# Kernel optimization log

Hardware: AMD Instinct MI355X
Metric: run time of the kernel (lower is better)

Reference implementation:

```python
import jax, jax.numpy as jnp
import numpy as np

B, L, H, N, NB = 16, 4096, 256, 64, 4
EXPAND = 2


def setup_inputs() -> dict:
    key = jax.random.key(0)
    ks = jax.random.split(key, 12)
    def nrm(k, shape, scale):
        return jax.random.normal(k, shape, dtype=jnp.float32) * scale
    inp = {}
    inp["x"] = jax.random.normal(ks[0], (B, L, 1), dtype=jnp.float32)
    # conv stem: Conv1d(1 -> H, kernel 5, pad 2)
    inp["conv_w"] = nrm(ks[1], (H, 1, 5), 1.0 / np.sqrt(5.0))
    inp["conv_b"] = jnp.zeros((H,), jnp.float32)
    # per-block S4 (S4D diagonal kernel) params, stacked over NB blocks
    inp["s4_norm_w"] = jnp.ones((NB, H), jnp.float32)
    inp["s4_norm_b"] = jnp.zeros((NB, H), jnp.float32)
    inp["log_dt"] = (np.log(0.001) + jax.random.uniform(ks[2], (NB, H), dtype=jnp.float32) * (np.log(0.1) - np.log(0.001))).astype(jnp.float32)
    inp["log_A_real"] = jnp.full((NB, H, N), np.log(0.5), jnp.float32)
    inp["A_imag"] = jnp.tile(np.pi * jnp.arange(N, dtype=jnp.float32), (NB, H, 1))
    inp["C_re"] = nrm(ks[3], (NB, H, N), 0.5 ** 0.5)
    inp["C_im"] = nrm(ks[4], (NB, H, N), 0.5 ** 0.5)
    inp["D"] = nrm(ks[5], (NB, H), 1.0)
    # S4 output GLU linear: H -> 2H, then glu -> H
    inp["s4_out_w"] = nrm(ks[6], (NB, 2 * H, H), 1.0 / np.sqrt(H))
    inp["s4_out_b"] = jnp.zeros((NB, 2 * H), jnp.float32)
    # FF block (expand=2)
    inp["ff_norm_w"] = jnp.ones((NB, H), jnp.float32)
    inp["ff_norm_b"] = jnp.zeros((NB, H), jnp.float32)
    inp["ff_w1"] = nrm(ks[7], (NB, EXPAND * H, H), 1.0 / np.sqrt(H))
    inp["ff_b1"] = jnp.zeros((NB, EXPAND * H), jnp.float32)
    inp["ff_w2"] = nrm(ks[8], (NB, H, EXPAND * H), 1.0 / np.sqrt(EXPAND * H))
    inp["ff_b2"] = jnp.zeros((NB, H), jnp.float32)
    return inp


def _ln_ch(x, w, b):
    # LayerNorm over channel dim of x: [B, H, L] (prenorm on transposed layout)
    mu = jnp.mean(x, axis=1, keepdims=True)
    var = jnp.mean((x - mu) ** 2, axis=1, keepdims=True)
    return (x - mu) * jax.lax.rsqrt(var + 1e-5) * w[None, :, None] + b[None, :, None]


def _s4d_kernel(log_dt, log_A_real, A_imag, C_re, C_im, Lk):
    # Diagonal SSM (S4D) convolution kernel, returns [H, Lk]
    dt = jnp.exp(log_dt)                       # [H]
    A = -jnp.exp(log_A_real) + 1j * A_imag     # [H, N]
    dtA = A * dt[:, None]                      # [H, N]
    C = (C_re + 1j * C_im) * (jnp.exp(dtA) - 1.0) / A
    V = jnp.exp(dtA[:, :, None] * jnp.arange(Lk, dtype=jnp.float32))  # [H, N, Lk]
    return 2.0 * jnp.einsum('hn,hnl->hl', C, V).real


def reference(x, conv_w, conv_b, s4_norm_w, s4_norm_b, log_dt, log_A_real, A_imag,
              C_re, C_im, D, s4_out_w, s4_out_b, ff_norm_w, ff_norm_b,
              ff_w1, ff_b1, ff_w2, ff_b2):
    u = jnp.transpose(x, (0, 2, 1))  # [B, 1, L]
    h = jax.lax.conv_general_dilated(u, conv_w, (1,), [(2, 2)],
                                     dimension_numbers=('NCH', 'OIH', 'NCH'))
    h = h + conv_b[None, :, None]    # [B, H, L]
    Lx = h.shape[-1]
    for i in range(NB):
        # --- S4 residual block (prenorm, FFT long conv, D-skip, GELU, GLU out) ---
        z = _ln_ch(h, s4_norm_w[i], s4_norm_b[i])
        k = _s4d_kernel(log_dt[i], log_A_real[i], A_imag[i], C_re[i], C_im[i], Lx)
        zf = jnp.fft.rfft(z, n=2 * Lx)
        kf = jnp.fft.rfft(k, n=2 * Lx)
        y = jnp.fft.irfft(zf * kf[None], n=2 * Lx)[..., :Lx]
        y = y + z * D[i][None, :, None]
        y = jax.nn.gelu(y, approximate=False)
        y2 = jnp.einsum('fh,bhl->bfl', s4_out_w[i], y) + s4_out_b[i][None, :, None]
        a, g = jnp.split(y2, 2, axis=1)
        h = h + a * jax.nn.sigmoid(g)
        # --- FF residual block (prenorm, pointwise MLP expand=2, GELU) ---
        z = _ln_ch(h, ff_norm_w[i], ff_norm_b[i])
        z = jax.nn.gelu(jnp.einsum('fh,bhl->bfl', ff_w1[i], z) + ff_b1[i][None, :, None], approximate=False)
        z = jnp.einsum('hf,bfl->bhl', ff_w2[i], z) + ff_b2[i][None, :, None]
        h = h + z
    return h[:, :, -1]  # [B, H]
```

## Files before the change

kernel.cpp:

```cpp
#include <hip/hip_runtime.h>
#include <math.h>

#define Bq 16
#define Lq 4096
#define Hq 256
#define Nq 64
#define NBq 4
#define F2q 512
#define BLq (Bq*Lq)

typedef __attribute__((ext_vector_type(8))) short short8;
typedef __attribute__((ext_vector_type(4))) float f32x4;

__device__ __forceinline__ unsigned short f2bf(float f){
  unsigned u = __float_as_uint(f);
  u = (u + 0x7fffu + ((u >> 16) & 1u)) >> 16;
  return (unsigned short)u;
}
__device__ __forceinline__ float bf2f(unsigned short u){
  return __uint_as_float(((unsigned)u) << 16);
}
__device__ __forceinline__ float gelu(float x){
  float u = 0.79788456f*x*(1.f + 0.044715f*x*x);
  float t = 1.f - __fdividef(2.f, 1.f + __expf(2.f*fabsf(u)));
  return 0.5f*x*(1.f + copysignf(t, u));
}

__device__ __forceinline__ void stage16(const void* g, void* l){
  __builtin_amdgcn_global_load_lds((const __attribute__((address_space(1))) void*)g,
                                   (__attribute__((address_space(3))) void*)l, 16, 0, 0);
}

__global__ __launch_bounds__(256) void k_convln(const float* __restrict__ x,
    const float* __restrict__ cw, const float* __restrict__ cb,
    float* __restrict__ h, float* __restrict__ mu, float* __restrict__ rstd){
  __shared__ float xs[260];
  __shared__ float cwS[Hq*5];
  __shared__ float cbS[Hq];
  const int b = blockIdx.x >> 4;
  const int l0 = (blockIdx.x & 15) * 256;
  const int tid = threadIdx.x;
  for (int i=tid; i<Hq*5; i+=256) cwS[i] = cw[i];
  cbS[tid] = cb[tid];
  {
    int gl = l0 + tid - 2;
    xs[tid] = (gl>=0 && gl<Lq) ? x[(size_t)b*Lq + gl] : 0.f;
    if (tid < 4){
      int gl2 = l0 + 254 + tid;
      xs[256+tid] = (gl2>=0 && gl2<Lq) ? x[(size_t)b*Lq + gl2] : 0.f;
    }
  }
  __syncthreads();
  float s0=0.f, s1=0.f;
  float* hp = h + (size_t)b*Hq*Lq + l0 + tid;
  for (int c=0;c<Hq;c++){
    float acc = cbS[c];
    #pragma unroll
    for (int k=0;k<5;k++) acc = fmaf(cwS[c*5+k], xs[tid+k], acc);
    hp[(size_t)c*Lq] = acc;
    s0 += acc; s1 = fmaf(acc, acc, s1);
  }
  int col = b*Lq + l0 + tid;
  float m = s0 * (1.0f/256.0f);
  float var = s1*(1.0f/256.0f) - m*m;
  mu[col] = m;
  rstd[col] = rsqrtf(fmaxf(var, 0.f) + 1e-5f);
}

__global__ __launch_bounds__(256) void k_s4pre(const float* __restrict__ log_dt,
    const float* __restrict__ lar, const float* __restrict__ aim,
    const float* __restrict__ cre, const float* __restrict__ cim,
    float* __restrict__ wre, float* __restrict__ wim,
    float* __restrict__ c2re, float* __restrict__ c2im){
  int idx = blockIdx.x*256 + threadIdx.x;
  int hh = (idx >> 6) & (Hq-1);
  int i = idx >> 14;
  float dt = expf(log_dt[i*Hq + hh]);
  float are = -expf(lar[idx]);
  float ai  = aim[idx];
  float dre = are*dt, dim = ai*dt;
  float er = expf(dre);
  float wr = er*cosf(dim), wi = er*sinf(dim);
  float nr = wr - 1.f, ni = wi;
  float den = are*are + ai*ai;
  float qre = (nr*are + ni*ai)/den;
  float qim = (ni*are - nr*ai)/den;
  float Cr = cre[idx], Ci = cim[idx];
  float cer = Cr*qre - Ci*qim;
  float cei = Cr*qim + Ci*qre;
  wre[idx] = wr; wim[idx] = wi;
  c2re[idx] = 2.f*cer; c2im[idx] = 2.f*cei;
}

__global__ __launch_bounds__(256) void k_cvtw(const float* __restrict__ s0,
    const float* __restrict__ s1, const float* __restrict__ s2,
    unsigned short* __restrict__ d0, unsigned short* __restrict__ d1,
    unsigned short* __restrict__ d2){
  int idx = blockIdx.x*256 + threadIdx.x;
  d0[idx] = f2bf(s0[idx]);
  d1[idx] = f2bf(s1[idx]);
  d2[idx] = f2bf(s2[idx]);
}

__global__ __launch_bounds__(64) void k_s4mat(const float* __restrict__ wre_,
    const float* __restrict__ wim_, const float* __restrict__ c2re_,
    const float* __restrict__ c2im_, const float* __restrict__ Dp,
    unsigned short* __restrict__ G, unsigned short* __restrict__ Wb,
    float* __restrict__ w64re_, float* __restrict__ w64im_){
  __shared__ float Kv[64];
  const int n = threadIdx.x;
  const int ch = blockIdx.x;
  const int pidx = ch*64 + n;
  const float wr = wre_[pidx], wi = wim_[pidx];
  const float cr = c2re_[pidx], ci = c2im_[pidx];
  unsigned short* Gb = G + (size_t)ch*64*192;
  unsigned short* Wbb = Wb + (size_t)ch*128*64;
  float pre = 1.f, pim = 0.f;
  for (int t=0;t<64;t++){
    float a = cr*pre - ci*pim;
    #pragma unroll
    for (int m=1;m<64;m<<=1) a += __shfl_xor(a, m, 64);
    if (n==0) Kv[t] = a;
    Wbb[n*64 + (63-t)] = f2bf(pre);
    Wbb[(64+n)*64 + (63-t)] = f2bf(pim);
    float qre = pre*wr - pim*wi;
    float qim = pre*wi + pim*wr;
    Gb[t*192 + 64 + n]  = f2bf(cr*qre - ci*qim);
    Gb[t*192 + 128 + n] = f2bf(-(cr*qim + ci*qre));
    pre = qre; pim = qim;
  }
  w64re_[pidx] = pre; w64im_[pidx] = pim;
  __syncthreads();
  float dv = Dp[ch];
  for (int t=0;t<64;t++){
    float kv = (n<=t) ? Kv[t-n] : 0.f;
    if (n==t) kv += dv;
    Gb[t*192 + n] = f2bf(kv);
  }
}

__global__ __launch_bounds__(256) void k_lnfin(const float2* __restrict__ stats,
    float* __restrict__ mu, float* __restrict__ rstd){
  int col = blockIdx.x*256 + threadIdx.x;
  float2 s = stats[col];
  float m = s.x * (1.0f/256.0f);
  float var = s.y*(1.0f/256.0f) - m*m;
  mu[col] = m;
  rstd[col] = rsqrtf(fmaxf(var, 0.f) + 1e-5f);
}

__global__ __launch_bounds__(256) void k_prep(const float* __restrict__ h,
    const float* __restrict__ mu, const float* __restrict__ rstd,
    const float* __restrict__ lnw_, const float* __restrict__ lnb_,
    unsigned short* __restrict__ U, int ib){
  int idx = blockIdx.x*256 + threadIdx.x;
  int l = (idx & 511) * 8;
  int ch = (idx >> 9) & (Hq-1);
  int b = idx >> 17;
  float lw = lnw_[ib*Hq+ch], lb = lnb_[ib*Hq+ch];
  const float* hp = h + (((size_t)(b*Hq+ch))<<12) + l;
  const float* mp = mu + ((size_t)b<<12) + l;
  const float* rp = rstd + ((size_t)b<<12) + l;
  unsigned ow[8];
  #pragma unroll
  for (int j=0;j<8;j++){
    float z = (hp[j]-mp[j])*rp[j]*lw + lb;
    ow[j] = f2bf(z);
  }
  uint4 o;
  o.x = ow[0] | (ow[1]<<16); o.y = ow[2] | (ow[3]<<16);
  o.z = ow[4] | (ow[5]<<16); o.w = ow[6] | (ow[7]<<16);
  unsigned short* up = U + ((size_t)ch*1024 + b*64 + (l>>6))*192 + (l&63);
  *(uint4*)up = o;
}

__global__ __launch_bounds__(256,2) void k_bgemm(const unsigned short* __restrict__ Wb,
    const unsigned short* __restrict__ U, unsigned short* __restrict__ Bb){
  __shared__ __align__(16) char smem[34816];
  unsigned short* Alds = (unsigned short*)smem;
  unsigned short* Blds = (unsigned short*)(smem+16384);
  const int tid = threadIdx.x;
  const int lam = tid & 63;
  const int wv = tid >> 6;
  const int wr = wv >> 1, wc = wv & 1;
  const int ch = blockIdx.x;
  const int bc0 = blockIdx.y * 128;
  const unsigned short* Wch = Wb + (size_t)ch*128*64;
  const unsigned short* Uch = U + (size_t)ch*1024*192;
  const int rbase = lam & 15;
  const int kg = lam >> 4;
  const int x7 = lam & 7;
  const int xo0 = ((kg) ^ x7) * 8;
  const int xo1 = ((4+kg) ^ x7) * 8;
  f32x4 acc[4][4] = {};
  #pragma unroll
  for (int c=0;c<4;c++){
    int si = c*256 + tid;
    int row = si >> 3, blk = si & 7;
    int sb = blk ^ (row & 7);
    stage16(Wch + row*64 + sb*8, &Alds[(c*256 + wv*64)*8]);
    stage16(Uch + (size_t)(bc0+row)*192 + sb*8, &Blds[(c*256 + wv*64)*8]);
  }
  __syncthreads();
  #pragma unroll
  for (int kk=0;kk<2;kk++){
    const int xo = kk ? xo1 : xo0;
    short8 af[4], wf[4];
    #pragma unroll
    for (int mf=0;mf<4;mf++)
      af[mf] = *(const short8*)&Alds[(wr*64 + mf*16 + rbase)*64 + xo];
    #pragma unroll
    for (int nf=0;nf<4;nf++)
      wf[nf] = *(const short8*)&Blds[(wc*64 + nf*16 + rbase)*64 + xo];
    #pragma unroll
    for (int mf=0;mf<4;mf++)
      #pragma unroll
      for (int nf=0;nf<4;nf++)
        acc[mf][nf] = __builtin_amdgcn_mfma_f32_16x16x32_bf16(af[mf], wf[nf], acc[mf][nf], 0,0,0);
  }
  __syncthreads();
  unsigned* tru = (unsigned*)smem;
  const int mg = lam >> 4;
  const int ncol = lam & 15;
  #pragma unroll
  for (int nf=0;nf<4;nf++){
    int bcl = wc*64 + nf*16 + ncol;
    #pragma unroll
    for (int mf=0;mf<4;mf++){
      int n2h = wr*32 + mf*8 + mg*2;
      tru[bcl*68 + n2h]     = (unsigned)f2bf(acc[mf][nf][0]) | ((unsigned)f2bf(acc[mf][nf][1])<<16);
      tru[bcl*68 + n2h + 1] = (unsigned)f2bf(acc[mf][nf][2]) | ((unsigned)f2bf(acc[mf][nf][3])<<16);
    }
  }
  __syncthreads();
  {
    int row = tid >> 1, half = tid & 1;
    const unsigned* src = tru + row*68 + half*32;
    unsigned short* dst = Bb + ((size_t)ch*1024 + bc0 + row)*128 + half*64;
    #pragma unroll
    for (int j=0;j<8;j++)
      *(uint4*)(dst + j*8) = *(const uint4*)(src + j*4);
  }
}

__global__ __launch_bounds__(256) void k_cscan(const unsigned short* __restrict__ Bb,
    const float* __restrict__ w64re_, const float* __restrict__ w64im_,
    unsigned short* __restrict__ U){
  const int wid = blockIdx.x*4 + (threadIdx.x >> 6);
  const int n = threadIdx.x & 63;
  const int ch = wid & (Hq-1);
  const int b = wid >> 8;
  const float wr = w64re_[ch*64 + n];
  const float wi = w64im_[ch*64 + n];
  const unsigned short* bp = Bb + ((size_t)ch*1024 + b*64)*128 + n;
  unsigned short* up = U + ((size_t)ch*1024 + b*64)*192;
  float sre = 0.f, sim = 0.f;
  for (int c=0;c<64;c++){
    up[c*192 + 64 + n]  = f2bf(sre);
    up[c*192 + 128 + n] = f2bf(sim);
    float br = bf2f(bp[c*128]), bi = bf2f(bp[c*128 + 64]);
    float t = fmaf(wr, sre, fmaf(-wi, sim, br));
    sim = fmaf(wr, sim, fmaf(wi, sre, bi));
    sre = t;
  }
}

__global__ __launch_bounds__(256,2) void k_ygemm(const unsigned short* __restrict__ G,
    const unsigned short* __restrict__ U, unsigned short* __restrict__ ybuf){
  __shared__ __align__(16) char smem[40960];
  unsigned short* Alds = (unsigned short*)smem;
  unsigned short* Blds = (unsigned short*)(smem + 8192);
  const int tid = threadIdx.x;
  const int lam = tid & 63;
  const int wv = tid >> 6;
  const int ch = blockIdx.x;
  const int col0 = blockIdx.y * 256;
  const unsigned short* Gch = G + (size_t)ch*64*192;
  const unsigned short* Uch = U + (size_t)ch*1024*192;
  const int rbase = lam & 15;
  const int kg = lam >> 4;
  const int x7 = lam & 7;
  const int xo0 = ((kg) ^ x7) * 8;
  const int xo1 = ((4+kg) ^ x7) * 8;
  f32x4 acc[4][4] = {};
  for (int ks=0;ks<3;ks++){
    const int k0 = ks*64;
    #pragma unroll
    for (int c=0;c<2;c++){
      int si = c*256 + tid;
      int row = si >> 3, blk = si & 7;
      int sb = blk ^ (row & 7);
      stage16(Gch + row*192 + k0 + sb*8, &Alds[(c*256 + wv*64)*8]);
    }
    #pragma unroll
    for (int c=0;c<8;c++){
      int si = c*256 + tid;
      int row = si >> 3, blk = si & 7;
      int sb = blk ^ (row & 7);
      stage16(Uch + (size_t)(col0+row)*192 + k0 + sb*8, &Blds[(c*256 + wv*64)*8]);
    }
    __syncthreads();
    #pragma unroll
    for (int kk=0;kk<2;kk++){
      const int xo = kk ? xo1 : xo0;
      short8 af[4], wf[4];
      #pragma unroll
      for (int mf=0;mf<4;mf++)
        af[mf] = *(const short8*)&Alds[(mf*16 + rbase)*64 + xo];
      #pragma unroll
      for (int nf=0;nf<4;nf++)
        wf[nf] = *(const short8*)&Blds[(wv*64 + nf*16 + rbase)*64 + xo];
      #pragma unroll
      for (int mf=0;mf<4;mf++)
        #pragma unroll
        for (int nf=0;nf<4;nf++)
          acc[mf][nf] = __builtin_amdgcn_mfma_f32_16x16x32_bf16(af[mf], wf[nf], acc[mf][nf], 0,0,0);
    }
    __syncthreads();
  }
  unsigned short* trans = (unsigned short*)smem + wv*64*66;
  const int mg = lam >> 4;
  const int ncol = lam & 15;
  #pragma unroll
  for (int mf=0;mf<4;mf++){
    #pragma unroll
    for (int nf=0;nf<4;nf++){
      #pragma unroll
      for (int r=0;r<4;r++){
        int l = mf*16 + mg*4 + r;
        int bcl = nf*16 + ncol;
        trans[bcl*66 + l] = f2bf(gelu(acc[mf][nf][r]));
      }
    }
  }
  __syncthreads();
  const int bc = col0 + wv*64 + lam;
  const int b = bc >> 6, c = bc & 63;
  unsigned short* yp = ybuf + (((size_t)(b*Hq + ch))<<12) + c*64;
  #pragma unroll
  for (int j=0;j<8;j++){
    uint4 v = *(const uint4*)&trans[lam*66 + j*8];
    *(uint4*)(yp + j*8) = v;
  }
}

__global__ __launch_bounds__(256) void k_transp(const unsigned short* __restrict__ src,
    unsigned short* __restrict__ dst){
  __shared__ unsigned lds[64][65];
  const int t = threadIdx.x;
  const int tile = blockIdx.x;
  const int l0 = (tile & 63)*64;
  const int c0 = ((tile>>6)&3)*64;
  const int b = tile >> 8;
  const int rr = t >> 3, c8 = t & 7;
  #pragma unroll
  for (int q=0;q<2;q++){
    int ch = rr + q*32;
    const unsigned short* sp = src + ((size_t)b*Hq + c0+ch)*Lq + l0 + c8*8;
    uint4 v = *(const uint4*)sp;
    lds[ch][c8*8+0] = v.x & 0xffff; lds[ch][c8*8+1] = v.x >> 16;
    lds[ch][c8*8+2] = v.y & 0xffff; lds[ch][c8*8+3] = v.y >> 16;
    lds[ch][c8*8+4] = v.z & 0xffff; lds[ch][c8*8+5] = v.z >> 16;
    lds[ch][c8*8+6] = v.w & 0xffff; lds[ch][c8*8+7] = v.w >> 16;
  }
  __syncthreads();
  #pragma unroll
  for (int q=0;q<2;q++){
    int l = rr + q*32;
    unsigned a[8];
    #pragma unroll
    for (int j=0;j<8;j++) a[j] = lds[c8*8+j][l];
    uint4 o;
    o.x = (a[0]&0xffff) | (a[1]<<16);
    o.y = (a[2]&0xffff) | (a[3]<<16);
    o.z = (a[4]&0xffff) | (a[5]<<16);
    o.w = (a[6]&0xffff) | (a[7]<<16);
    *(uint4*)(dst + ((size_t)b*Lq + l0+l)*Hq + c0 + c8*8) = o;
  }
}

__global__ __launch_bounds__(256) void k_lntransp(const float* __restrict__ h,
    const float* __restrict__ mu, const float* __restrict__ rstd,
    const float* __restrict__ lnw_, const float* __restrict__ lnb_,
    unsigned short* __restrict__ dst, int ib){
  __shared__ unsigned lds[64][65];
  const int t = threadIdx.x;
  const int tile = blockIdx.x;
  const int l0 = (tile & 63)*64;
  const int c0 = ((tile>>6)&3)*64;
  const int b = tile >> 8;
  const int rr = t >> 3, c8 = t & 7;
  #pragma unroll
  for (int q=0;q<2;q++){
    int ch = c0 + rr + q*32;
    float lw = lnw_[ib*Hq + ch], lb = lnb_[ib*Hq + ch];
    const float* sp = h + ((size_t)b*Hq + ch)*Lq + l0 + c8*8;
    const float* mp = mu + (size_t)b*Lq + l0 + c8*8;
    const float* rp = rstd + (size_t)b*Lq + l0 + c8*8;
    #pragma unroll
    for (int j=0;j<8;j++){
      float z = (sp[j] - mp[j]) * rp[j] * lw + lb;
      lds[rr + q*32][c8*8+j] = f2bf(z);
    }
  }
  __syncthreads();
  #pragma unroll
  for (int q=0;q<2;q++){
    int l = rr + q*32;
    unsigned a[8];
    #pragma unroll
    for (int j=0;j<8;j++) a[j] = lds[c8*8+j][l];
    uint4 o;
    o.x = (a[0]&0xffff) | (a[1]<<16);
    o.y = (a[2]&0xffff) | (a[3]<<16);
    o.z = (a[4]&0xffff) | (a[5]<<16);
    o.w = (a[6]&0xffff) | (a[7]<<16);
    *(uint4*)(dst + ((size_t)b*Lq + l0+l)*Hq + c0 + c8*8) = o;
  }
}

template<int MODE, int KDIM>
__global__ __launch_bounds__(256,2) void k_gemm(
    const unsigned short* __restrict__ A, const unsigned short* __restrict__ W,
    const float* __restrict__ bias, float* __restrict__ h,
    unsigned short* __restrict__ out, float2* __restrict__ stats){
  constexpr int WSH = (MODE==0?2:1)*128*64;
  constexpr int STG_B = (128*64 + WSH)*2;
  constexpr int EPI_B = (MODE==1) ? 128*136*2 : 64*132*4;
  constexpr int SMEM = STG_B > EPI_B ? STG_B : EPI_B;
  __shared__ __align__(16) char smem[SMEM];
  unsigned short* Alds = (unsigned short*)smem;
  unsigned short* Wlds = Alds + 128*64;
  const int tid = threadIdx.x;
  const int lam = tid & 63;
  const int wv = tid >> 6;
  const int wr = wv >> 1, wc = wv & 1;
  const int col0 = blockIdx.x * 128;
  const int n0 = blockIdx.y * 128;
  const int rbase = lam & 15;
  const int kg = lam >> 4;
  const int x7 = lam & 7;
  const int xo0 = ((kg) ^ x7) * 8;
  const int xo1 = ((4+kg) ^ x7) * 8;
  const unsigned short *aP[4], *wP[4], *wP2[4];
  unsigned sDst[4];
  #pragma unroll
  for (int c=0;c<4;c++){
    int si = c*256 + tid;
    int row = si >> 3, blk = si & 7;
    int sb = blk ^ (row & 7);
    aP[c] = A + (size_t)(col0+row)*KDIM + sb*8;
    wP[c] = W + (size_t)(n0+row)*KDIM + sb*8;
    wP2[c] = (MODE==0) ? (W + (size_t)(n0+256+row)*KDIM + sb*8) : nullptr;
    sDst[c] = (unsigned)(c*256 + wv*64)*8;
  }
  f32x4 acc[4][4] = {};
  f32x4 acc2[4][4] = {};
  for (int k0 = 0; k0 < KDIM; k0 += 64){
    #pragma unroll
    for (int c=0;c<4;c++){
      stage16(aP[c] + k0, &Alds[sDst[c]]);
      stage16(wP[c] + k0, &Wlds[sDst[c]]);
      if constexpr (MODE==0) stage16(wP2[c] + k0, &Wlds[8192 + sDst[c]]);
    }
    __syncthreads();
    #pragma unroll
    for (int kk=0;kk<2;kk++){
      const int xo = kk ? xo1 : xo0;
      short8 af[4], wf[4];
      #pragma unroll
      for (int mf=0;mf<4;mf++)
        af[mf] = *(const short8*)&Alds[(wr*64 + mf*16 + rbase)*64 + xo];
      #pragma unroll
      for (int nf=0;nf<4;nf++)
        wf[nf] = *(const short8*)&Wlds[(wc*64 + nf*16 + rbase)*64 + xo];
      if constexpr (MODE==0){
        short8 wg[4];
        #pragma unroll
        for (int nf=0;nf<4;nf++)
          wg[nf] = *(const short8*)&Wlds[8192 + (wc*64 + nf*16 + rbase)*64 + xo];
        #pragma unroll
        for (int mf=0;mf<4;mf++){
          #pragma unroll
          for (int nf=0;nf<4;nf++){
            acc[mf][nf]  = __builtin_amdgcn_mfma_f32_16x16x32_bf16(af[mf], wf[nf], acc[mf][nf], 0,0,0);
            acc2[mf][nf] = __builtin_amdgcn_mfma_f32_16x16x32_bf16(af[mf], wg[nf], acc2[mf][nf], 0,0,0);
          }
        }
      } else {
        #pragma unroll
        for (int mf=0;mf<4;mf++){
          #pragma unroll
          for (int nf=0;nf<4;nf++)
            acc[mf][nf] = __builtin_amdgcn_mfma_f32_16x16x32_bf16(af[mf], wf[nf], acc[mf][nf], 0,0,0);
        }
      }
    }
    __syncthreads();
  }
  const int mg = lam >> 4;
  const int ncol = lam & 15;
  if constexpr (MODE==1){
    unsigned short* trans = (unsigned short*)smem;
    #pragma unroll
    for (int nf=0;nf<4;nf++){
      int gnl = wc*64 + nf*16 + ncol;
      float bb1 = bias[n0 + gnl];
      #pragma unroll
      for (int mf=0;mf<4;mf++){
        int cl = wr*64 + mf*16 + mg*4;
        #pragma unroll
        for (int r=0;r<4;r++)
          trans[(cl+r)*136 + gnl] = f2bf(gelu(acc[mf][nf][r] + bb1));
      }
    }
    __syncthreads();
    {
      int cl = tid >> 1, gs = (tid & 1)*64;
      const unsigned short* src = trans + cl*136 + gs;
      unsigned short* dst = out + (size_t)(col0+cl)*F2q + n0 + gs;
      #pragma unroll
      for (int j=0;j<8;j++)
        *(uint4*)(dst + j*8) = *(const uint4*)(src + j*8);
    }
  } else {
    float* dlds = (float*)smem;
    const int bb = col0 >> 12;
    const int l0 = col0 & (Lq-1);
    #pragma unroll
    for (int p=0;p<2;p++){
      __syncthreads();
      if (wc == p){
        #pragma unroll
        for (int nf=0;nf<4;nf++){
          int chl = nf*16 + ncol;
          int gn = n0 + p*64 + chl;
          float ba = bias[gn];
          float bg = (MODE==0) ? bias[gn + Hq] : 0.f;
          #pragma unroll
          for (int mf=0;mf<4;mf++){
            int coll = wr*64 + mf*16 + mg*4;
            #pragma unroll
            for (int r=0;r<4;r++){
              float d;
              if constexpr (MODE==0){
                float av = acc[mf][nf][r] + ba;
                float gv = acc2[mf][nf][r] + bg;
                d = __fdividef(av, 1.f + __expf(-gv));
              } else {
                d = acc[mf][nf][r] + ba;
              }
              dlds[chl*132 + coll + r] = d;
            }
          }
        }
      }
      __syncthreads();
      {
        int chl = tid >> 2, lq = (tid & 3)*32;
        float* hp = h + ((size_t)bb*Hq + n0 + p*64 + chl)*Lq + l0 + lq;
        float* dp = dlds + chl*132 + lq;
        #pragma unroll
        for (int j=0;j<8;j++){
          f32x4 hv = *(f32x4*)(hp + j*4);
          f32x4 dv = *(const f32x4*)(dp + j*4);
          #pragma unroll
          for (int r=0;r<4;r++) hv[r] += dv[r];
          *(f32x4*)(hp + j*4) = hv;
          *(f32x4*)(dp + j*4) = hv;
        }
      }
      __syncthreads();
      {
        int j = tid >> 1, hc = (tid & 1)*32;
        float s0 = 0.f, s1 = 0.f;
        #pragma unroll
        for (int c=0;c<32;c++){
          float v = dlds[(hc+c)*132 + j];
          s0 += v; s1 = fmaf(v, v, s1);
        }
        s0 += __shfl_xor(s0, 1, 64);
        s1 += __shfl_xor(s1, 1, 64);
        if (!(tid & 1)){
          atomicAdd(&stats[col0 + j].x, s0);
          atomicAdd(&stats[col0 + j].y, s1);
        }
      }
    }
  }
}

__global__ __launch_bounds__(256) void k_gather(const float* __restrict__ h,
    float* __restrict__ o){
  int idx = blockIdx.x*256 + threadIdx.x;
  int b = idx >> 8, c = idx & (Hq-1);
  o[idx] = h[((size_t)b*Hq + c)*Lq + (Lq-1)];
}

extern "C" void kernel_launch(void* const* d_in, const int* in_sizes, int n_in,
                              void* d_out, int out_size, void* d_ws, size_t ws_size,
                              hipStream_t stream) {
  (void)in_sizes; (void)n_in; (void)out_size; (void)ws_size;
  const float* x         = (const float*)d_in[0];
  const float* conv_w    = (const float*)d_in[1];
  const float* conv_b    = (const float*)d_in[2];
  const float* s4_norm_w = (const float*)d_in[3];
  const float* s4_norm_b = (const float*)d_in[4];
  const float* log_dt    = (const float*)d_in[5];
  const float* log_A_real= (const float*)d_in[6];
  const float* A_imag    = (const float*)d_in[7];
  const float* C_re      = (const float*)d_in[8];
  const float* C_im      = (const float*)d_in[9];
  const float* Dp        = (const float*)d_in[10];
  const float* s4_out_w  = (const float*)d_in[11];
  const float* s4_out_b  = (const float*)d_in[12];
  const float* ff_norm_w = (const float*)d_in[13];
  const float* ff_norm_b = (const float*)d_in[14];
  const float* ff_w1     = (const float*)d_in[15];
  const float* ff_b1     = (const float*)d_in[16];
  const float* ff_w2     = (const float*)d_in[17];
  const float* ff_b2     = (const float*)d_in[18];

  char* ws = (char*)d_ws;
  size_t off = 0;
  auto nxt = [&](size_t bytes){ size_t o = off; off = (off + bytes + 255) & ~(size_t)255; return o; };
  float* h      = (float*)(ws + nxt((size_t)Bq*Hq*Lq*4));
  float* mu     = (float*)(ws + nxt((size_t)BLq*4));
  float* rstd   = (float*)(ws + nxt((size_t)BLq*4));
  float* wre    = (float*)(ws + nxt((size_t)NBq*Hq*Nq*4));
  float* wim    = (float*)(ws + nxt((size_t)NBq*Hq*Nq*4));
  float* c2re   = (float*)(ws + nxt((size_t)NBq*Hq*Nq*4));
  float* c2im   = (float*)(ws + nxt((size_t)NBq*Hq*Nq*4));
  float* w64re  = (float*)(ws + nxt((size_t)NBq*Hq*Nq*4));
  float* w64im  = (float*)(ws + nxt((size_t)NBq*Hq*Nq*4));
  unsigned short* s4wb = (unsigned short*)(ws + nxt((size_t)NBq*F2q*Hq*2));
  unsigned short* f1b  = (unsigned short*)(ws + nxt((size_t)NBq*F2q*Hq*2));
  unsigned short* f2b  = (unsigned short*)(ws + nxt((size_t)NBq*Hq*F2q*2));
  unsigned short* Gm   = (unsigned short*)(ws + nxt((size_t)Hq*64*192*2));
  unsigned short* Wbar = (unsigned short*)(ws + nxt((size_t)Hq*128*64*2));
  unsigned short* U    = (unsigned short*)(ws + nxt((size_t)Hq*1024*192*2));
  unsigned short* Bb   = (unsigned short*)(ws + nxt((size_t)Hq*128*1024*2));
  unsigned short* ybuf = Bb;
  unsigned short* yT   = Bb + (size_t)16*1024*1024;
  unsigned short* zT   = yT;
  unsigned short* z2T  = U;
  float2* stats = (float2*)Bb;

  k_convln<<<Bq*16, 256, 0, stream>>>(x, conv_w, conv_b, h, mu, rstd);
  k_s4pre<<<(NBq*Hq*Nq)/256, 256, 0, stream>>>(log_dt, log_A_real, A_imag, C_re, C_im,
                                               wre, wim, c2re, c2im);
  k_cvtw<<<(NBq*F2q*Hq)/256, 256, 0, stream>>>(s4_out_w, ff_w1, ff_w2, s4wb, f1b, f2b);

  for (int i=0;i<NBq;i++){
    const size_t po = (size_t)i*Hq*Nq;
    k_s4mat<<<Hq, 64, 0, stream>>>(wre+po, wim+po, c2re+po, c2im+po, Dp + i*Hq,
                                   Gm, Wbar, w64re+po, w64im+po);
    k_prep<<<(Bq*Hq*Lq/8)/256, 256, 0, stream>>>(h, mu, rstd, s4_norm_w, s4_norm_b, U, i);
    k_bgemm<<<dim3(Hq, 8), 256, 0, stream>>>(Wbar, U, Bb);
    k_cscan<<<(Bq*Hq)/4, 256, 0, stream>>>(Bb, w64re+po, w64im+po, U);
    k_ygemm<<<dim3(Hq, 4), 256, 0, stream>>>(Gm, U, ybuf);
    k_transp<<<Bq*4*64, 256, 0, stream>>>(ybuf, yT);
    hipMemsetAsync(stats, 0, (size_t)BLq*sizeof(float2), stream);
    k_gemm<0,256><<<dim3(BLq/128, 2), 256, 0, stream>>>(
        yT, s4wb + (size_t)i*F2q*Hq, s4_out_b + (size_t)i*F2q, h, nullptr, stats);
    k_lnfin<<<BLq/256, 256, 0, stream>>>(stats, mu, rstd);
    k_lntransp<<<Bq*4*64, 256, 0, stream>>>(h, mu, rstd, ff_norm_w, ff_norm_b, zT, i);
    k_gemm<1,256><<<dim3(BLq/128, 4), 256, 0, stream>>>(
        zT, f1b + (size_t)i*F2q*Hq, ff_b1 + (size_t)i*F2q, nullptr, z2T, nullptr);
    hipMemsetAsync(stats, 0, (size_t)BLq*sizeof(float2), stream);
    k_gemm<2,512><<<dim3(BLq/128, 2), 256, 0, stream>>>(
        z2T, f2b + (size_t)i*Hq*F2q, ff_b2 + (size_t)i*Hq, h, nullptr, stats);
    k_lnfin<<<BLq/256, 256, 0, stream>>>(stats, mu, rstd);
  }
  k_gather<<<(Bq*Hq)/256, 256, 0, stream>>>(h, (float*)d_out);
}
```

Baseline: 1.333 ms.

## Widen FF GEMM N-tiles and fuse LayerNorm stats into second FF GEMM

The FF GEMMs now use 256-wide output tiles. The first FF GEMM runs on half as many blocks, each loading the A tile once for twice the outputs. The second FF GEMM covers all 256 channels per block, so it can compute per-column mean and rstd directly. This removes the stats memset, the atomics and the separate LN-finalize kernel. The epilogue LDS layout is padded differently to cut bank conflicts. In exchange, accumulator register pressure doubles and the grid is smaller, which may hurt occupancy.

```diff
diff --git a/kernel.cpp b/kernel.cpp
--- a/kernel.cpp
+++ b/kernel.cpp
@@ -423,11 +423,12 @@
 __global__ __launch_bounds__(256,2) void k_gemm(
     const unsigned short* __restrict__ A, const unsigned short* __restrict__ W,
     const float* __restrict__ bias, float* __restrict__ h,
-    unsigned short* __restrict__ out, float2* __restrict__ stats){
-  constexpr int WSH = (MODE==0?2:1)*128*64;
-  constexpr int STG_B = (128*64 + WSH)*2;
-  constexpr int EPI_B = (MODE==1) ? 128*136*2 : 64*132*4;
-  constexpr int SMEM = STG_B > EPI_B ? STG_B : EPI_B;
+    unsigned short* __restrict__ out, float2* __restrict__ stats,
+    float* __restrict__ mu, float* __restrict__ rstd){
+  constexpr int NT = (MODE==0) ? 128 : 256;
+  constexpr int NF = NT/32;
+  constexpr int WCG = NT/2;
+  constexpr int SMEM = 49152;
   __shared__ __align__(16) char smem[SMEM];
   unsigned short* Alds = (unsigned short*)smem;
   unsigned short* Wlds = Alds + 128*64;
@@ -436,13 +437,13 @@
   const int wv = tid >> 6;
   const int wr = wv >> 1, wc = wv & 1;
   const int col0 = blockIdx.x * 128;
-  const int n0 = blockIdx.y * 128;
+  const int n0 = blockIdx.y * NT;
   const int rbase = lam & 15;
   const int kg = lam >> 4;
   const int x7 = lam & 7;
   const int xo0 = ((kg) ^ x7) * 8;
   const int xo1 = ((4+kg) ^ x7) * 8;
-  const unsigned short *aP[4], *wP[4], *wP2[4];
+  const unsigned short *aP[4], *wP[8], *wP2[4];
   unsigned sDst[4];
   #pragma unroll
   for (int c=0;c<4;c++){
@@ -450,30 +451,47 @@
     int row = si >> 3, blk = si & 7;
     int sb = blk ^ (row & 7);
     aP[c] = A + (size_t)(col0+row)*KDIM + sb*8;
-    wP[c] = W + (size_t)(n0+row)*KDIM + sb*8;
-    wP2[c] = (MODE==0) ? (W + (size_t)(n0+256+row)*KDIM + sb*8) : nullptr;
     sDst[c] = (unsigned)(c*256 + wv*64)*8;
-  }
-  f32x4 acc[4][4] = {};
-  f32x4 acc2[4][4] = {};
+    if constexpr (MODE==0){
+      wP[c]  = W + (size_t)(n0+row)*KDIM + sb*8;
+      wP2[c] = W + (size_t)(n0+256+row)*KDIM + sb*8;
+    }
+  }
+  if constexpr (MODE!=0){
+    #pragma unroll
+    for (int c=0;c<8;c++){
+      int si = c*256 + tid;
+      int row = si >> 3, blk = si & 7;
+      int sb = blk ^ (row & 7);
+      wP[c] = W + (size_t)(n0+row)*KDIM + sb*8;
+    }
+  }
+  f32x4 acc[4][NF] = {};
+  f32x4 acc2[4][(MODE==0)?4:1] = {};
   for (int k0 = 0; k0 < KDIM; k0 += 64){
     #pragma unroll
-    for (int c=0;c<4;c++){
-      stage16(aP[c] + k0, &Alds[sDst[c]]);
-      stage16(wP[c] + k0, &Wlds[sDst[c]]);
-      if constexpr (MODE==0) stage16(wP2[c] + k0, &Wlds[8192 + sDst[c]]);
+    for (int c=0;c<4;c++) stage16(aP[c] + k0, &Alds[sDst[c]]);
+    if constexpr (MODE==0){
+      #pragma unroll
+      for (int c=0;c<4;c++){
+        stage16(wP[c] + k0, &Wlds[sDst[c]]);
+        stage16(wP2[c] + k0, &Wlds[8192 + sDst[c]]);
+      }
+    } else {
+      #pragma unroll
+      for (int c=0;c<8;c++) stage16(wP[c] + k0, &Wlds[(c*256 + wv*64)*8]);
     }
     __syncthreads();
     #pragma unroll
     for (int kk=0;kk<2;kk++){
       const int xo = kk ? xo1 : xo0;
-      short8 af[4], wf[4];
+      short8 af[4], wf[NF];
       #pragma unroll
       for (int mf=0;mf<4;mf++)
         af[mf] = *(const short8*)&Alds[(wr*64 + mf*16 + rbase)*64 + xo];
       #pragma unroll
-      for (int nf=0;nf<4;nf++)
-        wf[nf] = *(const short8*)&Wlds[(wc*64 + nf*16 + rbase)*64 + xo];
+      for (int nf=0;nf<NF;nf++)
+        wf[nf] = *(const short8*)&Wlds[(wc*WCG + nf*16 + rbase)*64 + xo];
       if constexpr (MODE==0){
         short8 wg[4];
         #pragma unroll
@@ -491,7 +509,7 @@
         #pragma unroll
         for (int mf=0;mf<4;mf++){
           #pragma unroll
-          for (int nf=0;nf<4;nf++)
+          for (int nf=0;nf<NF;nf++)
             acc[mf][nf] = __builtin_amdgcn_mfma_f32_16x16x32_bf16(af[mf], wf[nf], acc[mf][nf], 0,0,0);
         }
       }
@@ -503,63 +521,73 @@
   if constexpr (MODE==1){
     unsigned short* trans = (unsigned short*)smem;
     #pragma unroll
-    for (int nf=0;nf<4;nf++){
-      int gnl = wc*64 + nf*16 + ncol;
-      float bb1 = bias[n0 + gnl];
-      #pragma unroll
-      for (int mf=0;mf<4;mf++){
-        int cl = wr*64 + mf*16 + mg*4;
-        #pragma unroll
-        for (int r=0;r<4;r++)
-          trans[(cl+r)*136 + gnl] = f2bf(gelu(acc[mf][nf][r] + bb1));
-      }
-    }
-    __syncthreads();
-    {
-      int cl = tid >> 1, gs = (tid & 1)*64;
-      const unsigned short* src = trans + cl*136 + gs;
-      unsigned short* dst = out + (size_t)(col0+cl)*F2q + n0 + gs;
-      #pragma unroll
-      for (int j=0;j<8;j++)
-        *(uint4*)(dst + j*8) = *(const uint4*)(src + j*8);
+    for (int gh=0; gh<2; gh++){
+      __syncthreads();
+      if (wc == gh){
+        #pragma unroll
+        for (int nf=0;nf<8;nf++){
+          int gnl = nf*16 + ncol;
+          float bb1 = bias[n0 + gh*128 + gnl];
+          #pragma unroll
+          for (int mf=0;mf<4;mf++){
+            int cl = wr*64 + mf*16 + mg*4;
+            #pragma unroll
+            for (int r=0;r<4;r++)
+              trans[(cl+r)*136 + gnl] = f2bf(gelu(acc[mf][nf][r] + bb1));
+          }
+        }
+      }
+      __syncthreads();
+      {
+        int cl = tid >> 1, gs = (tid & 1)*64;
+        const unsigned short* src = trans + cl*136 + gs;
+        unsigned short* dst = out + (size_t)(col0+cl)*F2q + n0 + gh*128 + gs;
+        #pragma unroll
+        for (int j=0;j<8;j++)
+          *(uint4*)(dst + j*8) = *(const uint4*)(src + j*8);
+      }
     }
   } else {
     float* dlds = (float*)smem;
     const int bb = col0 >> 12;
     const int l0 = col0 & (Lq-1);
-    #pragma unroll
-    for (int p=0;p<2;p++){
+    constexpr int NPASS = (MODE==0) ? 2 : 4;
+    float s0t = 0.f, s1t = 0.f;
+    #pragma unroll
+    for (int p=0;p<NPASS;p++){
       __syncthreads();
-      if (wc == p){
-        #pragma unroll
-        for (int nf=0;nf<4;nf++){
-          int chl = nf*16 + ncol;
+      const int owner = (MODE==0) ? p : (p>>1);
+      const int nfb = (MODE==0) ? 0 : (p&1)*4;
+      if (wc == owner){
+        #pragma unroll
+        for (int nf2=0;nf2<4;nf2++){
+          int chl = nf2*16 + ncol;
           int gn = n0 + p*64 + chl;
           float ba = bias[gn];
           float bg = (MODE==0) ? bias[gn + Hq] : 0.f;
           #pragma unroll
           for (int mf=0;mf<4;mf++){
             int coll = wr*64 + mf*16 + mg*4;
+            f32x4 dv;
             #pragma unroll
             for (int r=0;r<4;r++){
-              float d;
               if constexpr (MODE==0){
-                float av = acc[mf][nf][r] + ba;
-                float gv = acc2[mf][nf][r] + bg;
-                d = __fdividef(av, 1.f + __expf(-gv));
+                float av = acc[mf][nfb+nf2][r] + ba;
+                float gv = acc2[mf][nf2][r] + bg;
+                dv[r] = __fdividef(av, 1.f + __expf(-gv));
               } else {
-                d = acc[mf][nf][r] + ba;
+                dv[r] = acc[mf][nfb+nf2][r] + ba;
               }
-              dlds[chl*132 + coll + r] = d;
             }
+            *(f32x4*)&dlds[chl*144 + (coll>>5)*36 + (coll&31)] = dv;
           }
         }
       }
       __syncthreads();
       {
-        int chl = tid >> 2, lq = (tid & 3)*32;
-        float* hp = h + ((size_t)bb*Hq + n0 + p*64 + chl)*Lq + l0 + lq;
-        float* dp = dlds + chl*132 + lq;
+        int chl = tid >> 2, seg = tid & 3;
+        float* hp = h + ((size_t)bb*Hq + n0 + p*64 + chl)*Lq + l0 + seg*32;
+        float* dp = dlds + chl*144 + seg*36;
         #pragma unroll
         for (int j=0;j<8;j++){
           f32x4 hv = *(f32x4*)(hp + j*4);
@@ -573,18 +601,34 @@
       __syncthreads();
       {
         int j = tid >> 1, hc = (tid & 1)*32;
+        int js = (j>>5)*36 + (j&31);
         float s0 = 0.f, s1 = 0.f;
         #pragma unroll
         for (int c=0;c<32;c++){
-          float v = dlds[(hc+c)*132 + j];
+          float v = dlds[(hc+c)*144 + js];
           s0 += v; s1 = fmaf(v, v, s1);
         }
-        s0 += __shfl_xor(s0, 1, 64);
-        s1 += __shfl_xor(s1, 1, 64);
-        if (!(tid & 1)){
-          atomicAdd(&stats[col0 + j].x, s0);
-          atomicAdd(&stats[col0 + j].y, s1);
+        if constexpr (MODE==0){
+          s0 += __shfl_xor(s0, 1, 64);
+          s1 += __shfl_xor(s1, 1, 64);
+          if (!(tid & 1)){
+            atomicAdd(&stats[col0 + j].x, s0);
+            atomicAdd(&stats[col0 + j].y, s1);
+          }
+        } else {
+          s0t += s0; s1t += s1;
         }
+      }
+    }
+    if constexpr (MODE==2){
+      s0t += __shfl_xor(s0t, 1, 64);
+      s1t += __shfl_xor(s1t, 1, 64);
+      if (!(tid & 1)){
+        int col = col0 + (tid >> 1);
+        float m = s0t * (1.0f/256.0f);
+        float var = s1t*(1.0f/256.0f) - m*m;
+        mu[col] = m;
+        rstd[col] = rsqrtf(fmaxf(var, 0.f) + 1e-5f);
       }
     }
   }
@@ -662,15 +706,16 @@
     k_transp<<<Bq*4*64, 256, 0, stream>>>(ybuf, yT);
     hipMemsetAsync(stats, 0, (size_t)BLq*sizeof(float2), stream);
     k_gemm<0,256><<<dim3(BLq/128, 2), 256, 0, stream>>>(
-        yT, s4wb + (size_t)i*F2q*Hq, s4_out_b + (size_t)i*F2q, h, nullptr, stats);
+        yT, s4wb + (size_t)i*F2q*Hq, s4_out_b + (size_t)i*F2q, h, nullptr, stats,
+        nullptr, nullptr);
     k_lnfin<<<BLq/256, 256, 0, stream>>>(stats, mu, rstd);
     k_lntransp<<<Bq*4*64, 256, 0, stream>>>(h, mu, rstd, ff_norm_w, ff_norm_b, zT, i);
-    k_gemm<1,256><<<dim3(BLq/128, 4), 256, 0, stream>>>(
-        zT, f1b + (size_t)i*F2q*Hq, ff_b1 + (size_t)i*F2q, nullptr, z2T, nullptr);
-    hipMemsetAsync(stats, 0, (size_t)BLq*sizeof(float2), stream);
-    k_gemm<2,512><<<dim3(BLq/128, 2), 256, 0, stream>>>(
-        z2T, f2b + (size_t)i*Hq*F2q, ff_b2 + (size_t)i*Hq, h, nullptr, stats);
-    k_lnfin<<<BLq/256, 256, 0, stream>>>(stats, mu, rstd);
+    k_gemm<1,256><<<dim3(BLq/128, 2), 256, 0, stream>>>(
+        zT, f1b + (size_t)i*F2q*Hq, ff_b1 + (size_t)i*F2q, nullptr, z2T, nullptr,
+        nullptr, nullptr);
+    k_gemm<2,512><<<dim3(BLq/128, 1), 256, 0, stream>>>(
+        z2T, f2b + (size_t)i*Hq*F2q, ff_b2 + (size_t)i*Hq, h, nullptr, nullptr,
+        mu, rstd);
   }
   k_gather<<<(Bq*Hq)/256, 256, 0, stream>>>(h, (float*)d_out);
 }
```

After: 1.369 ms. +2.7%, slower.

## Store residual stream h in bf16 instead of fp32

Applied to the files above, without the earlier changes.

The residual stream h is now kept as bf16 in every kernel that touches it: conv stem, LayerNorm prep, transpose, GEMM epilogue residual add, and gather. This halves the HBM traffic for h, which is read and rewritten many times per block. The epilogue LDS stride also changes to a padded 144/36 layout so each lane can write one f32x4, and the unused acc2 array is shrunk for MODE 1. The cost is accuracy: residual sums are rounded to bf16 after every block, and that error compounds across the layers.

```diff
diff --git a/kernel.cpp b/kernel.cpp
--- a/kernel.cpp
+++ b/kernel.cpp
@@ -33,7 +33,7 @@
 
 __global__ __launch_bounds__(256) void k_convln(const float* __restrict__ x,
     const float* __restrict__ cw, const float* __restrict__ cb,
-    float* __restrict__ h, float* __restrict__ mu, float* __restrict__ rstd){
+    unsigned short* __restrict__ h, float* __restrict__ mu, float* __restrict__ rstd){
   __shared__ float xs[260];
   __shared__ float cwS[Hq*5];
   __shared__ float cbS[Hq];
@@ -52,12 +52,12 @@
   }
   __syncthreads();
   float s0=0.f, s1=0.f;
-  float* hp = h + (size_t)b*Hq*Lq + l0 + tid;
+  unsigned short* hp = h + (size_t)b*Hq*Lq + l0 + tid;
   for (int c=0;c<Hq;c++){
     float acc = cbS[c];
     #pragma unroll
     for (int k=0;k<5;k++) acc = fmaf(cwS[c*5+k], xs[tid+k], acc);
-    hp[(size_t)c*Lq] = acc;
+    hp[(size_t)c*Lq] = f2bf(acc);
     s0 += acc; s1 = fmaf(acc, acc, s1);
   }
   int col = b*Lq + l0 + tid;
@@ -149,7 +149,7 @@
   rstd[col] = rsqrtf(fmaxf(var, 0.f) + 1e-5f);
 }
 
-__global__ __launch_bounds__(256) void k_prep(const float* __restrict__ h,
+__global__ __launch_bounds__(256) void k_prep(const unsigned short* __restrict__ h,
     const float* __restrict__ mu, const float* __restrict__ rstd,
     const float* __restrict__ lnw_, const float* __restrict__ lnb_,
     unsigned short* __restrict__ U, int ib){
@@ -158,13 +158,19 @@
   int ch = (idx >> 9) & (Hq-1);
   int b = idx >> 17;
   float lw = lnw_[ib*Hq+ch], lb = lnb_[ib*Hq+ch];
-  const float* hp = h + (((size_t)(b*Hq+ch))<<12) + l;
+  const unsigned short* hp = h + (((size_t)(b*Hq+ch))<<12) + l;
   const float* mp = mu + ((size_t)b<<12) + l;
   const float* rp = rstd + ((size_t)b<<12) + l;
+  uint4 hv = *(const uint4*)hp;
+  float hf[8];
+  hf[0]=bf2f(hv.x&0xffff); hf[1]=bf2f(hv.x>>16);
+  hf[2]=bf2f(hv.y&0xffff); hf[3]=bf2f(hv.y>>16);
+  hf[4]=bf2f(hv.z&0xffff); hf[5]=bf2f(hv.z>>16);
+  hf[6]=bf2f(hv.w&0xffff); hf[7]=bf2f(hv.w>>16);
   unsigned ow[8];
   #pragma unroll
   for (int j=0;j<8;j++){
-    float z = (hp[j]-mp[j])*rp[j]*lw + lb;
+    float z = (hf[j]-mp[j])*rp[j]*lw + lb;
     ow[j] = f2bf(z);
   }
   uint4 o;
@@ -379,7 +385,7 @@
   }
 }
 
-__global__ __launch_bounds__(256) void k_lntransp(const float* __restrict__ h,
+__global__ __launch_bounds__(256) void k_lntransp(const unsigned short* __restrict__ h,
     const float* __restrict__ mu, const float* __restrict__ rstd,
     const float* __restrict__ lnw_, const float* __restrict__ lnb_,
     unsigned short* __restrict__ dst, int ib){
@@ -394,12 +400,18 @@
   for (int q=0;q<2;q++){
     int ch = c0 + rr + q*32;
     float lw = lnw_[ib*Hq + ch], lb = lnb_[ib*Hq + ch];
-    const float* sp = h + ((size_t)b*Hq + ch)*Lq + l0 + c8*8;
+    const unsigned short* sp = h + ((size_t)b*Hq + ch)*Lq + l0 + c8*8;
     const float* mp = mu + (size_t)b*Lq + l0 + c8*8;
     const float* rp = rstd + (size_t)b*Lq + l0 + c8*8;
+    uint4 hv = *(const uint4*)sp;
+    float hf[8];
+    hf[0]=bf2f(hv.x&0xffff); hf[1]=bf2f(hv.x>>16);
+    hf[2]=bf2f(hv.y&0xffff); hf[3]=bf2f(hv.y>>16);
+    hf[4]=bf2f(hv.z&0xffff); hf[5]=bf2f(hv.z>>16);
+    hf[6]=bf2f(hv.w&0xffff); hf[7]=bf2f(hv.w>>16);
     #pragma unroll
     for (int j=0;j<8;j++){
-      float z = (sp[j] - mp[j]) * rp[j] * lw + lb;
+      float z = (hf[j] - mp[j]) * rp[j] * lw + lb;
       lds[rr + q*32][c8*8+j] = f2bf(z);
     }
   }
@@ -422,11 +434,11 @@
 template<int MODE, int KDIM>
 __global__ __launch_bounds__(256,2) void k_gemm(
     const unsigned short* __restrict__ A, const unsigned short* __restrict__ W,
-    const float* __restrict__ bias, float* __restrict__ h,
+    const float* __restrict__ bias, unsigned short* __restrict__ h,
     unsigned short* __restrict__ out, float2* __restrict__ stats){
   constexpr int WSH = (MODE==0?2:1)*128*64;
   constexpr int STG_B = (128*64 + WSH)*2;
-  constexpr int EPI_B = (MODE==1) ? 128*136*2 : 64*132*4;
+  constexpr int EPI_B = (MODE==1) ? 128*136*2 : 64*144*4;
   constexpr int SMEM = STG_B > EPI_B ? STG_B : EPI_B;
   __shared__ __align__(16) char smem[SMEM];
   unsigned short* Alds = (unsigned short*)smem;
@@ -455,7 +467,7 @@
     sDst[c] = (unsigned)(c*256 + wv*64)*8;
   }
   f32x4 acc[4][4] = {};
-  f32x4 acc2[4][4] = {};
+  f32x4 acc2[4][(MODE==0)?4:1] = {};
   for (int k0 = 0; k0 < KDIM; k0 += 64){
     #pragma unroll
     for (int c=0;c<4;c++){
@@ -540,43 +552,52 @@
           #pragma unroll
           for (int mf=0;mf<4;mf++){
             int coll = wr*64 + mf*16 + mg*4;
+            f32x4 dv;
             #pragma unroll
             for (int r=0;r<4;r++){
-              float d;
               if constexpr (MODE==0){
                 float av = acc[mf][nf][r] + ba;
                 float gv = acc2[mf][nf][r] + bg;
-                d = __fdividef(av, 1.f + __expf(-gv));
+                dv[r] = __fdividef(av, 1.f + __expf(-gv));
               } else {
-                d = acc[mf][nf][r] + ba;
+                dv[r] = acc[mf][nf][r] + ba;
               }
-              dlds[chl*132 + coll + r] = d;
             }
+            *(f32x4*)&dlds[chl*144 + (coll>>5)*36 + (coll&31)] = dv;
           }
         }
       }
       __syncthreads();
       {
-        int chl = tid >> 2, lq = (tid & 3)*32;
-        float* hp = h + ((size_t)bb*Hq + n0 + p*64 + chl)*Lq + l0 + lq;
-        float* dp = dlds + chl*132 + lq;
-        #pragma unroll
-        for (int j=0;j<8;j++){
-          f32x4 hv = *(f32x4*)(hp + j*4);
-          f32x4 dv = *(const f32x4*)(dp + j*4);
-          #pragma unroll
-          for (int r=0;r<4;r++) hv[r] += dv[r];
-          *(f32x4*)(hp + j*4) = hv;
-          *(f32x4*)(dp + j*4) = hv;
+        int chl = tid >> 2, seg = tid & 3;
+        unsigned short* hp = h + ((size_t)bb*Hq + n0 + p*64 + chl)*Lq + l0 + seg*32;
+        float* dp = dlds + chl*144 + seg*36;
+        #pragma unroll
+        for (int j=0;j<4;j++){
+          uint4 hv = *(uint4*)(hp + j*8);
+          f32x4 d0 = *(const f32x4*)(dp + j*8);
+          f32x4 d1 = *(const f32x4*)(dp + j*8 + 4);
+          d0[0] += bf2f(hv.x&0xffff); d0[1] += bf2f(hv.x>>16);
+          d0[2] += bf2f(hv.y&0xffff); d0[3] += bf2f(hv.y>>16);
+          d1[0] += bf2f(hv.z&0xffff); d1[1] += bf2f(hv.z>>16);
+          d1[2] += bf2f(hv.w&0xffff); d1[3] += bf2f(hv.w>>16);
+          hv.x = (unsigned)f2bf(d0[0]) | ((unsigned)f2bf(d0[1])<<16);
+          hv.y = (unsigned)f2bf(d0[2]) | ((unsigned)f2bf(d0[3])<<16);
+          hv.z = (unsigned)f2bf(d1[0]) | ((unsigned)f2bf(d1[1])<<16);
+          hv.w = (unsigned)f2bf(d1[2]) | ((unsigned)f2bf(d1[3])<<16);
+          *(uint4*)(hp + j*8) = hv;
+          *(f32x4*)(dp + j*8) = d0;
+          *(f32x4*)(dp + j*8 + 4) = d1;
         }
       }
       __syncthreads();
       {
         int j = tid >> 1, hc = (tid & 1)*32;
+        int js = (j>>5)*36 + (j&31);
         float s0 = 0.f, s1 = 0.f;
         #pragma unroll
         for (int c=0;c<32;c++){
-          float v = dlds[(hc+c)*132 + j];
+          float v = dlds[(hc+c)*144 + js];
           s0 += v; s1 = fmaf(v, v, s1);
         }
         s0 += __shfl_xor(s0, 1, 64);
@@ -590,11 +611,11 @@
   }
 }
 
-__global__ __launch_bounds__(256) void k_gather(const float* __restrict__ h,
+__global__ __launch_bounds__(256) void k_gather(const unsigned short* __restrict__ h,
     float* __restrict__ o){
   int idx = blockIdx.x*256 + threadIdx.x;
   int b = idx >> 8, c = idx & (Hq-1);
-  o[idx] = h[((size_t)b*Hq + c)*Lq + (Lq-1)];
+  o[idx] = bf2f(h[((size_t)b*Hq + c)*Lq + (Lq-1)]);
 }
 
 extern "C" void kernel_launch(void* const* d_in, const int* in_sizes, int n_in,
@@ -624,7 +645,7 @@
   char* ws = (char*)d_ws;
   size_t off = 0;
   auto nxt = [&](size_t bytes){ size_t o = off; off = (off + bytes + 255) & ~(size_t)255; return o; };
-  float* h      = (float*)(ws + nxt((size_t)Bq*Hq*Lq*4));
+  unsigned short* h = (unsigned short*)(ws + nxt((size_t)Bq*Hq*Lq*2));
   float* mu     = (float*)(ws + nxt((size_t)BLq*4));
   float* rstd   = (float*)(ws + nxt((size_t)BLq*4));
   float* wre    = (float*)(ws + nxt((size_t)NBq*Hq*Nq*4));
```

Result: faster. 1.212 ms (-9.1%).
